# Performance work log

Hardware: AMD Instinct MI355X
Metric: run time of the kernel (lower is better)

Reference implementation:

```python
import jax, jax.numpy as jnp
import numpy as np

B, S, E = 2, 2048, 2048
H = 16
KV_RANK = 512
ROPE = 64
NOPE = 64  # source sets qk_nope_dim = qk_rope_dim
VD = 128   # v_head_dim = head_dim
QD = ROPE + NOPE  # q_head_dim = 128


def setup_inputs() -> dict:
    key = jax.random.key(0)
    ks = jax.random.split(key, 5)
    sd = lambda fan_in: 1.0 / np.sqrt(fan_in)
    return {
        "x": jax.random.normal(ks[0], (B, S, E), jnp.float32),
        "attention_mask": jnp.zeros((1, 1, S, S), jnp.float32),
        "W_kv_down": jax.random.normal(ks[1], (KV_RANK + ROPE, E), jnp.float32) * sd(E),
        "W_kv_up": jax.random.normal(ks[2], (H * (VD + NOPE), KV_RANK), jnp.float32) * sd(KV_RANK),
        "W_q": jax.random.normal(ks[3], (H * QD, E), jnp.float32) * sd(E),
        "W_out": jax.random.normal(ks[4], (E, H * VD), jnp.float32) * sd(H * VD),
    }


def reference(x, attention_mask, W_kv_down, W_kv_up, W_q, W_out):
    scale = QD ** (-0.5)
    # down-project to latent + rope part
    compressed = jnp.einsum('bse,fe->bsf', x, W_kv_down)          # [B,S,KV_RANK+ROPE]
    kv_c, k_rope = compressed[..., :KV_RANK], compressed[..., KV_RANK:]
    # up-project latent to per-head v and k_nope
    kv_exp = jnp.einsum('bsr,fr->bsf', kv_c, W_kv_up)             # [B,S,H*(VD+NOPE)]
    kv_exp = kv_exp.reshape(B, S, H, VD + NOPE).transpose(0, 2, 1, 3)  # [B,H,S,VD+NOPE]
    v, k_nope = kv_exp[..., :VD], kv_exp[..., VD:]
    # shared rope key broadcast over heads, concat [rope, nope]
    k_rope_b = jnp.broadcast_to(k_rope[:, None], (B, H, S, ROPE))
    k = jnp.concatenate([k_rope_b, k_nope], axis=-1)              # [B,H,S,QD]
    # queries
    q = jnp.einsum('bse,fe->bsf', x, W_q).reshape(B, S, H, QD).transpose(0, 2, 1, 3)
    scores = jnp.einsum('bhsd,bhtd->bhst', q, k) * scale + attention_mask
    w = jax.nn.softmax(scores, axis=-1)
    out = jnp.einsum('bhst,bhtv->bhsv', w, v)                     # [B,H,S,VD]
    out = out.transpose(0, 2, 1, 3).reshape(B, S, H * VD)
    return jnp.einsum('bsf,ef->bse', out, W_out)
```

## Files before the change

### kernel.cpp

```cpp
#include <hip/hip_runtime.h>
#include <hip/hip_bf16.h>
#include <stdint.h>

typedef __bf16 bf16x8 __attribute__((ext_vector_type(8)));
typedef float f32x4 __attribute__((ext_vector_type(4)));
typedef float f32x16 __attribute__((ext_vector_type(16)));
typedef uint32_t u32x4 __attribute__((ext_vector_type(4)));
typedef unsigned short ushort_t;
typedef unsigned short ushort8v __attribute__((ext_vector_type(8)));

#define MFMA16 __builtin_amdgcn_mfma_f32_16x16x32_bf16
#define MFMA32 __builtin_amdgcn_mfma_f32_32x32x16_bf16

static constexpr int Bc = 2, Sc = 2048, Ec = 2048, Hc = 16;

__device__ __forceinline__ void gload16(const void* g, void* l) {
  __builtin_amdgcn_global_load_lds(
      (const __attribute__((address_space(1))) void*)g,
      (__attribute__((address_space(3))) void*)l, 16, 0, 0);
}

__device__ __forceinline__ ushort_t f2bf(float f) {
  uint32_t u = __float_as_uint(f);
  uint32_t r = (u + 0x7fffu + ((u >> 16) & 1u)) >> 16;
  return (ushort_t)r;
}
__device__ __forceinline__ float bf2f(ushort_t u) {
  return __uint_as_float((uint32_t)u << 16);
}
__device__ __forceinline__ uint32_t cvtpk(float a, float b) {
  uint32_t d;
  asm("v_cvt_pk_bf16_f32 %0, %1, %2" : "=v"(d) : "v"(a), "v"(b));
  return d;
}
__device__ __forceinline__ void plswap(uint32_t& a, uint32_t& b) {
  asm("v_permlane32_swap_b32 %0, %1" : "+v"(a), "+v"(b));
}

__global__ void cast_all(const float* __restrict__ x, const float* __restrict__ Wq,
                         const float* __restrict__ Wkvu, const float* __restrict__ Wout,
                         const float* __restrict__ Wkvd,
                         ushort_t* __restrict__ xb, ushort_t* __restrict__ wq,
                         ushort_t* __restrict__ wkvu, ushort_t* __restrict__ wout,
                         ushort_t* __restrict__ wkvd) {
  int i = blockIdx.x * 256 + threadIdx.x;
  const float* src;
  ushort_t* dst;
  int j;
  if (i < 2097152) { src = x; dst = xb; j = i; }
  else if (i < 3145728) { src = Wq; dst = wq; j = i - 2097152; }
  else if (i < 3538944) { src = Wkvu; dst = wkvu; j = i - 3145728; }
  else if (i < 4587520) { src = Wout; dst = wout; j = i - 3538944; }
  else {
    j = i - 4587520;
    int row = j >> 9, col4 = j & 511;
    ushort4 o;
    if (row < 576) {
      float4 v = ((const float4*)Wkvd)[row * 512 + col4];
      o.x = f2bf(v.x); o.y = f2bf(v.y); o.z = f2bf(v.z); o.w = f2bf(v.w);
    } else { o.x = 0; o.y = 0; o.z = 0; o.w = 0; }
    ((ushort4*)wkvd)[j] = o;
    return;
  }
  float4 v = ((const float4*)src)[j];
  ushort4 o;
  o.x = f2bf(v.x); o.y = f2bf(v.y); o.z = f2bf(v.z); o.w = f2bf(v.w);
  ((ushort4*)dst)[j] = o;
}

__global__ void mask_rearrange(const float* __restrict__ mask, ushort_t* __restrict__ m4) {
  const float INVLN2 = 1.4426950408889634f;
  int i = blockIdx.x * 256 + threadIdx.x;
  if (i >= 524288) return;
  int rr = i & 1, half = (i >> 1) & 1, kblk = (i >> 2) & 1, kt = (i >> 3) & 31, q = i >> 8;
  const float* src = mask + (size_t)q * 2048 + kt * 64 + kblk * 32 + half * 4 + rr * 16;
  float4 a = *(const float4*)src;
  float4 c = *(const float4*)(src + 8);
  ushort8v o;
  o[0] = f2bf(a.x * INVLN2); o[1] = f2bf(a.y * INVLN2);
  o[2] = f2bf(a.z * INVLN2); o[3] = f2bf(a.w * INVLN2);
  o[4] = f2bf(c.x * INVLN2); o[5] = f2bf(c.y * INVLN2);
  o[6] = f2bf(c.z * INVLN2); o[7] = f2bf(c.w * INVLN2);
  ((ushort8v*)m4)[i] = o;
}

template<int MODE>
__global__ __launch_bounds__(256, 2)
void gemm_bt(const ushort_t* __restrict__ A, int lda,
             const ushort_t* __restrict__ Bm, int ldb,
             void* __restrict__ Cout, int ldc,
             int M, int N, int K,
             char* __restrict__ vtb, char* __restrict__ kbuf)
{
  __shared__ __align__(16) ushort_t sA[128 * 32];
  __shared__ __align__(16) ushort_t sB[128 * 32];
  int tid = threadIdx.x;
  int nTn = N >> 7;
  int bid = blockIdx.x;
  int chunk = gridDim.x >> 3;
  bid = (bid & 7) * chunk + (bid >> 3);
  int tm = bid / nTn, tn = bid - tm * nTn;
  int wave = tid >> 6, lane = tid & 63;
  int wm = (wave >> 1) << 6, wn = (wave & 1) << 6;
  int l16 = lane & 15, g16 = lane >> 4;
  f32x4 acc[4][4] = {};
  int srow = tid >> 2, scol = (tid & 3) << 3;
  const ushort_t* Ag = A + (size_t)(tm * 128 + srow) * lda + scol;
  const ushort_t* Bg = Bm + (size_t)(tn * 128 + srow) * ldb + scol;
  ushort_t* sAp = &sA[srow * 32 + scol];
  ushort_t* sBp = &sB[srow * 32 + scol];
  for (int kt = 0; kt < K; kt += 32) {
    gload16(Ag, sAp);
    gload16(Ag + (size_t)64 * lda, sAp + 64 * 32);
    gload16(Bg, sBp);
    gload16(Bg + (size_t)64 * ldb, sBp + 64 * 32);
    Ag += 32; Bg += 32;
    __syncthreads();
    bf16x8 af[4], bfr[4];
#pragma unroll
    for (int i = 0; i < 4; i++) af[i] = *(const bf16x8*)&sA[(wm + i * 16 + l16) * 32 + g16 * 8];
#pragma unroll
    for (int i = 0; i < 4; i++) bfr[i] = *(const bf16x8*)&sB[(wn + i * 16 + l16) * 32 + g16 * 8];
#pragma unroll
    for (int i = 0; i < 4; i++)
#pragma unroll
      for (int j = 0; j < 4; j++)
        acc[i][j] = MFMA16(af[i], bfr[j], acc[i][j], 0, 0, 0);
    __syncthreads();
  }
#pragma unroll
  for (int i = 0; i < 4; i++) {
#pragma unroll
    for (int j = 0; j < 4; j++) {
#pragma unroll
      for (int r = 0; r < 4; r++) {
        int grow = tm * 128 + wm + i * 16 + g16 * 4 + r;
        int gcol = tn * 128 + wn + j * 16 + l16;
        float v = acc[i][j][r];
        if constexpr (MODE == 0) {
          ((ushort_t*)Cout)[(size_t)grow * ldc + gcol] = f2bf(v);
        } else if constexpr (MODE == 2) {
          ((float*)Cout)[(size_t)grow * ldc + gcol] = v;
        } else {
          int h = gcol / 192, jj = gcol - h * 192;
          int b = grow >> 11, s = grow & 2047;
          size_t bh = (size_t)(b * Hc + h);
          if (jj < 128) {
            *(ushort_t*)(vtb + bh * 524288 + (size_t)jj * 4096 + ((s >> 6) * 128) +
                         ((2 * (s & 63)) ^ ((jj & 7) << 4))) = f2bf(v);
          } else {
            int col = 64 + (jj - 128);
            *(ushort_t*)(kbuf + (bh * Sc + s) * 256 + ((2 * col) ^ ((s & 7) << 4))) = f2bf(v);
          }
        }
      }
    }
  }
}

__global__ void rope_fill(const ushort_t* __restrict__ comp, char* __restrict__ kbuf) {
  int i = blockIdx.x * 256 + threadIdx.x;
  if (i >= Bc * Sc * 8) return;
  int blk = i & 7;
  int m = i >> 3;
  int s = m & 2047, b = m >> 11;
  uint4 v = *(const uint4*)&comp[(size_t)m * 640 + 512 + blk * 8];
  int off = (blk * 16) ^ ((s & 7) << 4);
#pragma unroll
  for (int h = 0; h < Hc; h++) {
    *(uint4*)(kbuf + ((size_t)(b * Hc + h) * Sc + s) * 256 + off) = v;
  }
}

__global__ __launch_bounds__(128, 2)
void attn_kernel(const ushort_t* __restrict__ qb, const char* __restrict__ kbuf,
                 const char* __restrict__ vtb, const ushort_t* __restrict__ m4,
                 ushort_t* __restrict__ attn_o)
{
  __shared__ __align__(16) char smem[32768];
  char* sK = smem;
  char* sV = smem + 16384;
  const float scale2 = 0.12752081738040466f;
  int bid = blockIdx.x;
  bid = (bid & 7) * 128 + (bid >> 3);
  int qt = bid & 31, bh = bid >> 5;
  int b = bh >> 4, h = bh & 15;
  int tid = threadIdx.x, wave = tid >> 6, lane = tid & 63;
  int l32 = lane & 31, half = lane >> 5;
  int sx = (l32 & 7) << 4;
  int qbase = qt * 64 + wave * 32;

  bf16x8 qf[8];
  {
    const ushort_t* qp = qb + (size_t)(b * Sc + qbase + l32) * 2048 + h * 128 + half * 8;
#pragma unroll
    for (int ks = 0; ks < 8; ks++) qf[ks] = *(const bf16x8*)(qp + ks * 16);
  }

  float mrun = -3.0e38f, lrun = 0.f;
  f32x16 acco[4] = {};

  const char* kg = kbuf + (size_t)bh * 524288;
  const char* vg = vtb + (size_t)bh * 524288;
  const ushort8v* mq = (const ushort8v*)m4 + (size_t)(qbase + l32) * 256 + half * 2;

  for (int kt = 0; kt < 32; kt++) {
#pragma unroll
    for (int it = 0; it < 8; it++)
      gload16(kg + kt * 16384 + it * 2048 + tid * 16, sK + it * 2048 + tid * 16);
#pragma unroll
    for (int it = 0; it < 8; it++) {
      int l = it * 2048 + tid * 16;
      gload16(vg + (size_t)(l >> 7) * 4096 + kt * 128 + (l & 127), sV + l);
    }
    ushort8v mvv[4];
#pragma unroll
    for (int kb = 0; kb < 2; kb++)
#pragma unroll
      for (int rr = 0; rr < 2; rr++)
        mvv[kb * 2 + rr] = mq[kt * 8 + kb * 4 + rr];
    __syncthreads();

#pragma unroll
    for (int kblk = 0; kblk < 2; kblk++) {
      f32x16 sc = {};
      __builtin_amdgcn_s_setprio(1);
#pragma unroll
      for (int ks = 0; ks < 8; ks++) {
        bf16x8 kfr = *(const bf16x8*)(sK + (kblk * 32 + l32) * 256 +
                                      ((ks * 32 + half * 16) ^ sx));
        sc = MFMA32(kfr, qf[ks], sc, 0, 0, 0);
      }
      __builtin_amdgcn_s_setprio(0);

#pragma unroll
      for (int r = 0; r < 16; r++)
        sc[r] = sc[r] * scale2 + bf2f(mvv[kblk * 2 + (r >> 3)][r & 7]);
      float mx = sc[0];
#pragma unroll
      for (int r = 1; r < 16; r++) mx = fmaxf(mx, sc[r]);
      mx = fmaxf(mx, __shfl_xor(mx, 32));
      if (!__all(mx <= mrun + 11.0f)) {
        float mnew = fmaxf(mrun, mx);
        float corr = __builtin_amdgcn_exp2f(mrun - mnew);
        lrun *= corr; mrun = mnew;
#pragma unroll
        for (int r = 0; r < 16; r++) {
          float cr = __shfl(corr, (r & 3) + 8 * (r >> 2) + 4 * half);
#pragma unroll
          for (int vb = 0; vb < 4; vb++) acco[vb][r] *= cr;
        }
      }
      float rs = 0.f;
      uint32_t W[8];
#pragma unroll
      for (int m = 0; m < 4; m++) {
        float p0 = __builtin_amdgcn_exp2f(sc[4 * m + 0] - mrun);
        float p1 = __builtin_amdgcn_exp2f(sc[4 * m + 1] - mrun);
        float p2 = __builtin_amdgcn_exp2f(sc[4 * m + 2] - mrun);
        float p3 = __builtin_amdgcn_exp2f(sc[4 * m + 3] - mrun);
        rs += (p0 + p1) + (p2 + p3);
        W[2 * m] = cvtpk(p0, p1);
        W[2 * m + 1] = cvtpk(p2, p3);
      }
      lrun += rs;

      bf16x8 pf[2];
#pragma unroll
      for (int k2 = 0; k2 < 2; k2++) {
        uint32_t a0 = W[4 * k2 + 0], a1 = W[4 * k2 + 1];
        uint32_t b0 = W[4 * k2 + 2], b1 = W[4 * k2 + 3];
        plswap(a0, b0);
        plswap(a1, b1);
        u32x4 t; t[0] = a0; t[1] = a1; t[2] = b0; t[3] = b1;
        pf[k2] = __builtin_bit_cast(bf16x8, t);
      }

      __builtin_amdgcn_s_setprio(1);
#pragma unroll
      for (int k2 = 0; k2 < 2; k2++)
#pragma unroll
        for (int vb = 0; vb < 4; vb++) {
          bf16x8 vf = *(const bf16x8*)(sV + (vb * 32 + l32) * 128 +
                                       ((kblk * 64 + k2 * 32 + half * 16) ^ sx));
          acco[vb] = MFMA32(pf[k2], vf, acco[vb], 0, 0, 0);
        }
      __builtin_amdgcn_s_setprio(0);
    }

    __syncthreads();
  }

  lrun += __shfl_xor(lrun, 32);
#pragma unroll
  for (int r = 0; r < 16; r++) {
    int rowq = (r & 3) + 8 * (r >> 2) + 4 * half;
    float lr = __shfl(lrun, rowq);
    float inv = 1.0f / lr;
    int qrow = qbase + rowq;
    ushort_t* op = attn_o + (size_t)(b * Sc + qrow) * 2048 + h * 128 + l32;
#pragma unroll
    for (int vb = 0; vb < 4; vb++)
      op[vb * 32] = f2bf(acco[vb][r] * inv);
  }
}

extern "C" void kernel_launch(void* const* d_in, const int* in_sizes, int n_in,
                              void* d_out, int out_size, void* d_ws, size_t ws_size,
                              hipStream_t stream) {
  const float* x    = (const float*)d_in[0];
  const float* mask = (const float*)d_in[1];
  const float* Wkvd = (const float*)d_in[2];
  const float* Wkvu = (const float*)d_in[3];
  const float* Wq   = (const float*)d_in[4];
  const float* Wout = (const float*)d_in[5];

  char* ws = (char*)d_ws;
  size_t off = 0;
  auto alloc = [&](size_t bytes) { char* p = ws + off; off += (bytes + 255) & ~(size_t)255; return p; };
  ushort_t* xb   = (ushort_t*)alloc((size_t)4096 * 2048 * 2);
  ushort_t* wkvd = (ushort_t*)alloc((size_t)640 * 2048 * 2);
  ushort_t* wq   = (ushort_t*)alloc((size_t)2048 * 2048 * 2);
  ushort_t* wkvu = (ushort_t*)alloc((size_t)3072 * 512 * 2);
  ushort_t* wout = (ushort_t*)alloc((size_t)2048 * 2048 * 2);
  ushort_t* comp = (ushort_t*)alloc((size_t)4096 * 640 * 2);
  ushort_t* qbuf = (ushort_t*)alloc((size_t)4096 * 2048 * 2);
  char*     kbuf = alloc((size_t)Bc * Hc * Sc * 256);
  char*     vtb  = alloc((size_t)Bc * Hc * 524288);
  ushort_t* attn_o = xb;
  ushort_t* m4 = wq;

  cast_all<<<19200, 256, 0, stream>>>(x, Wq, Wkvu, Wout, Wkvd, xb, wq, wkvu, wout, wkvd);

  gemm_bt<0><<<32 * 5, 256, 0, stream>>>(xb, 2048, wkvd, 2048, comp, 640, 4096, 640, 2048, nullptr, nullptr);
  gemm_bt<0><<<32 * 16, 256, 0, stream>>>(xb, 2048, wq, 2048, qbuf, 2048, 4096, 2048, 2048, nullptr, nullptr);
  mask_rearrange<<<2048, 256, 0, stream>>>(mask, m4);
  gemm_bt<1><<<32 * 24, 256, 0, stream>>>(comp, 640, wkvu, 512, nullptr, 0, 4096, 3072, 512, vtb, kbuf);
  rope_fill<<<32768 / 256, 256, 0, stream>>>(comp, kbuf);
  attn_kernel<<<1024, 128, 0, stream>>>(qbuf, kbuf, vtb, m4, attn_o);
  gemm_bt<2><<<32 * 16, 256, 0, stream>>>(attn_o, 2048, wout, 2048, d_out, 2048, 4096, 2048, 2048, nullptr, nullptr);
}
```

Baseline: 288.9 us.

## Double-buffer K/V tiles in LDS and process 64 keys per softmax step

The attention kernel now allocates two LDS buffers for K and V, so the async global-to-LDS load of the next tile is issued before computing on the current one, overlapping memory with MFMA work. The two 32-key sub-blocks are also merged into one online-softmax update per 64-key tile, halving the max/rescale passes. LDS use doubles to 64KB per block, which may cut occupancy from the requested 2 blocks per CU. The larger live register set from two score tiles also risks spills.

```diff
diff --git a/kernel.cpp b/kernel.cpp
--- a/kernel.cpp
+++ b/kernel.cpp
@@ -177,9 +177,11 @@
                  const char* __restrict__ vtb, const ushort_t* __restrict__ m4,
                  ushort_t* __restrict__ attn_o)
 {
-  __shared__ __align__(16) char smem[32768];
-  char* sK = smem;
-  char* sV = smem + 16384;
+  __shared__ __align__(16) char smem[65536];
+  char* sKA = smem;
+  char* sVA = smem + 16384;
+  char* sKB = smem + 32768;
+  char* sVB = smem + 49152;
   const float scale2 = 0.12752081738040466f;
   int bid = blockIdx.x;
   bid = (bid & 7) * 128 + (bid >> 3);
@@ -204,90 +206,120 @@
   const char* vg = vtb + (size_t)bh * 524288;
   const ushort8v* mq = (const ushort8v*)m4 + (size_t)(qbase + l32) * 256 + half * 2;
 
-  for (int kt = 0; kt < 32; kt++) {
+  auto STAGE = [&](int kt, char* sKb, char* sVb) {
 #pragma unroll
     for (int it = 0; it < 8; it++)
-      gload16(kg + kt * 16384 + it * 2048 + tid * 16, sK + it * 2048 + tid * 16);
+      gload16(kg + kt * 16384 + it * 2048 + tid * 16, sKb + it * 2048 + tid * 16);
 #pragma unroll
     for (int it = 0; it < 8; it++) {
       int l = it * 2048 + tid * 16;
-      gload16(vg + (size_t)(l >> 7) * 4096 + kt * 128 + (l & 127), sV + l);
-    }
+      gload16(vg + (size_t)(l >> 7) * 4096 + kt * 128 + (l & 127), sVb + l);
+    }
+  };
+
+  auto COMPUTE = [&](int kt, const char* sKb, const char* sVb) {
     ushort8v mvv[4];
 #pragma unroll
     for (int kb = 0; kb < 2; kb++)
 #pragma unroll
       for (int rr = 0; rr < 2; rr++)
         mvv[kb * 2 + rr] = mq[kt * 8 + kb * 4 + rr];
+
+    f32x16 sc0 = {}, sc1 = {};
+    __builtin_amdgcn_s_setprio(1);
+#pragma unroll
+    for (int ks = 0; ks < 8; ks++) {
+      bf16x8 k0 = *(const bf16x8*)(sKb + l32 * 256 + ((ks * 32 + half * 16) ^ sx));
+      bf16x8 k1 = *(const bf16x8*)(sKb + (32 + l32) * 256 + ((ks * 32 + half * 16) ^ sx));
+      sc0 = MFMA32(k0, qf[ks], sc0, 0, 0, 0);
+      sc1 = MFMA32(k1, qf[ks], sc1, 0, 0, 0);
+    }
+    __builtin_amdgcn_s_setprio(0);
+
+#pragma unroll
+    for (int r = 0; r < 16; r++) {
+      sc0[r] = sc0[r] * scale2 + bf2f(mvv[r >> 3][r & 7]);
+      sc1[r] = sc1[r] * scale2 + bf2f(mvv[2 + (r >> 3)][r & 7]);
+    }
+    float mx = fmaxf(sc0[0], sc1[0]);
+#pragma unroll
+    for (int r = 1; r < 16; r++) mx = fmaxf(mx, fmaxf(sc0[r], sc1[r]));
+    mx = fmaxf(mx, __shfl_xor(mx, 32));
+    if (!__all(mx <= mrun + 11.0f)) {
+      float mnew = fmaxf(mrun, mx);
+      float corr = __builtin_amdgcn_exp2f(mrun - mnew);
+      lrun *= corr; mrun = mnew;
+#pragma unroll
+      for (int r = 0; r < 16; r++) {
+        float cr = __shfl(corr, (r & 3) + 8 * (r >> 2) + 4 * half);
+#pragma unroll
+        for (int vb = 0; vb < 4; vb++) acco[vb][r] *= cr;
+      }
+    }
+    float rs = 0.f;
+    uint32_t W0[8], W1[8];
+#pragma unroll
+    for (int m = 0; m < 4; m++) {
+      float a0 = __builtin_amdgcn_exp2f(sc0[4 * m + 0] - mrun);
+      float a1 = __builtin_amdgcn_exp2f(sc0[4 * m + 1] - mrun);
+      float a2 = __builtin_amdgcn_exp2f(sc0[4 * m + 2] - mrun);
+      float a3 = __builtin_amdgcn_exp2f(sc0[4 * m + 3] - mrun);
+      float b0 = __builtin_amdgcn_exp2f(sc1[4 * m + 0] - mrun);
+      float b1 = __builtin_amdgcn_exp2f(sc1[4 * m + 1] - mrun);
+      float b2 = __builtin_amdgcn_exp2f(sc1[4 * m + 2] - mrun);
+      float b3 = __builtin_amdgcn_exp2f(sc1[4 * m + 3] - mrun);
+      rs += (a0 + a1) + (a2 + a3) + (b0 + b1) + (b2 + b3);
+      W0[2 * m] = cvtpk(a0, a1); W0[2 * m + 1] = cvtpk(a2, a3);
+      W1[2 * m] = cvtpk(b0, b1); W1[2 * m + 1] = cvtpk(b2, b3);
+    }
+    lrun += rs;
+
+    bf16x8 pf0[2], pf1[2];
+#pragma unroll
+    for (int k2 = 0; k2 < 2; k2++) {
+      {
+        uint32_t a0 = W0[4 * k2 + 0], a1 = W0[4 * k2 + 1];
+        uint32_t b0 = W0[4 * k2 + 2], b1 = W0[4 * k2 + 3];
+        plswap(a0, b0); plswap(a1, b1);
+        u32x4 t; t[0] = a0; t[1] = a1; t[2] = b0; t[3] = b1;
+        pf0[k2] = __builtin_bit_cast(bf16x8, t);
+      }
+      {
+        uint32_t a0 = W1[4 * k2 + 0], a1 = W1[4 * k2 + 1];
+        uint32_t b0 = W1[4 * k2 + 2], b1 = W1[4 * k2 + 3];
+        plswap(a0, b0); plswap(a1, b1);
+        u32x4 t; t[0] = a0; t[1] = a1; t[2] = b0; t[3] = b1;
+        pf1[k2] = __builtin_bit_cast(bf16x8, t);
+      }
+    }
+
+    __builtin_amdgcn_s_setprio(1);
+#pragma unroll
+    for (int k2 = 0; k2 < 2; k2++) {
+#pragma unroll
+      for (int vb = 0; vb < 4; vb++) {
+        bf16x8 vf = *(const bf16x8*)(sVb + (vb * 32 + l32) * 128 +
+                                     ((k2 * 32 + half * 16) ^ sx));
+        acco[vb] = MFMA32(pf0[k2], vf, acco[vb], 0, 0, 0);
+      }
+#pragma unroll
+      for (int vb = 0; vb < 4; vb++) {
+        bf16x8 vf = *(const bf16x8*)(sVb + (vb * 32 + l32) * 128 +
+                                     ((64 + k2 * 32 + half * 16) ^ sx));
+        acco[vb] = MFMA32(pf1[k2], vf, acco[vb], 0, 0, 0);
+      }
+    }
+    __builtin_amdgcn_s_setprio(0);
+  };
+
+  STAGE(0, sKA, sVA);
+  __syncthreads();
+  for (int kt = 0; kt < 32; kt += 2) {
+    STAGE(kt + 1, sKB, sVB);
+    COMPUTE(kt, sKA, sVA);
     __syncthreads();
-
-#pragma unroll
-    for (int kblk = 0; kblk < 2; kblk++) {
-      f32x16 sc = {};
-      __builtin_amdgcn_s_setprio(1);
-#pragma unroll
-      for (int ks = 0; ks < 8; ks++) {
-        bf16x8 kfr = *(const bf16x8*)(sK + (kblk * 32 + l32) * 256 +
-                                      ((ks * 32 + half * 16) ^ sx));
-        sc = MFMA32(kfr, qf[ks], sc, 0, 0, 0);
-      }
-      __builtin_amdgcn_s_setprio(0);
-
-#pragma unroll
-      for (int r = 0; r < 16; r++)
-        sc[r] = sc[r] * scale2 + bf2f(mvv[kblk * 2 + (r >> 3)][r & 7]);
-      float mx = sc[0];
-#pragma unroll
-      for (int r = 1; r < 16; r++) mx = fmaxf(mx, sc[r]);
-      mx = fmaxf(mx, __shfl_xor(mx, 32));
-      if (!__all(mx <= mrun + 11.0f)) {
-        float mnew = fmaxf(mrun, mx);
-        float corr = __builtin_amdgcn_exp2f(mrun - mnew);
-        lrun *= corr; mrun = mnew;
-#pragma unroll
-        for (int r = 0; r < 16; r++) {
-          float cr = __shfl(corr, (r & 3) + 8 * (r >> 2) + 4 * half);
-#pragma unroll
-          for (int vb = 0; vb < 4; vb++) acco[vb][r] *= cr;
-        }
-      }
-      float rs = 0.f;
-      uint32_t W[8];
-#pragma unroll
-      for (int m = 0; m < 4; m++) {
-        float p0 = __builtin_amdgcn_exp2f(sc[4 * m + 0] - mrun);
-        float p1 = __builtin_amdgcn_exp2f(sc[4 * m + 1] - mrun);
-        float p2 = __builtin_amdgcn_exp2f(sc[4 * m + 2] - mrun);
-        float p3 = __builtin_amdgcn_exp2f(sc[4 * m + 3] - mrun);
-        rs += (p0 + p1) + (p2 + p3);
-        W[2 * m] = cvtpk(p0, p1);
-        W[2 * m + 1] = cvtpk(p2, p3);
-      }
-      lrun += rs;
-
-      bf16x8 pf[2];
-#pragma unroll
-      for (int k2 = 0; k2 < 2; k2++) {
-        uint32_t a0 = W[4 * k2 + 0], a1 = W[4 * k2 + 1];
-        uint32_t b0 = W[4 * k2 + 2], b1 = W[4 * k2 + 3];
-        plswap(a0, b0);
-        plswap(a1, b1);
-        u32x4 t; t[0] = a0; t[1] = a1; t[2] = b0; t[3] = b1;
-        pf[k2] = __builtin_bit_cast(bf16x8, t);
-      }
-
-      __builtin_amdgcn_s_setprio(1);
-#pragma unroll
-      for (int k2 = 0; k2 < 2; k2++)
-#pragma unroll
-        for (int vb = 0; vb < 4; vb++) {
-          bf16x8 vf = *(const bf16x8*)(sV + (vb * 32 + l32) * 128 +
-                                       ((kblk * 64 + k2 * 32 + half * 16) ^ sx));
-          acco[vb] = MFMA32(pf[k2], vf, acco[vb], 0, 0, 0);
-        }
-      __builtin_amdgcn_s_setprio(0);
-    }
-
+    if (kt + 2 < 32) STAGE(kt + 2, sKA, sVA);
+    COMPUTE(kt + 1, sKB, sVB);
     __syncthreads();
   }
 
```

Result: slower. 311.1 us (+7.7%).

## Process two 32-row query blocks per wave in attention to reuse K/V tiles

Applied to the files above, without the earlier changes.

Each attention wave now handles 64 query rows (two independent 32-row accumulators) instead of 32, so each block covers 128 queries and the grid halves to 512 blocks. Every K and V fragment read from shared memory feeds two MFMAs, which halves the global-to-LDS traffic and LDS reads per unit of work. In exchange register pressure roughly doubles, so launch bounds drop to one block per SM hint. Fewer blocks and fewer resident waves may expose more latency and leave the GPU underfilled.

```diff
diff --git a/kernel.cpp b/kernel.cpp
--- a/kernel.cpp
+++ b/kernel.cpp
@@ -172,7 +172,7 @@
   }
 }
 
-__global__ __launch_bounds__(128, 2)
+__global__ __launch_bounds__(128, 1)
 void attn_kernel(const ushort_t* __restrict__ qb, const char* __restrict__ kbuf,
                  const char* __restrict__ vtb, const ushort_t* __restrict__ m4,
                  ushort_t* __restrict__ attn_o)
@@ -182,27 +182,34 @@
   char* sV = smem + 16384;
   const float scale2 = 0.12752081738040466f;
   int bid = blockIdx.x;
-  bid = (bid & 7) * 128 + (bid >> 3);
-  int qt = bid & 31, bh = bid >> 5;
+  bid = (bid & 7) * 64 + (bid >> 3);
+  int qt = bid & 15, bh = bid >> 4;
   int b = bh >> 4, h = bh & 15;
   int tid = threadIdx.x, wave = tid >> 6, lane = tid & 63;
   int l32 = lane & 31, half = lane >> 5;
   int sx = (l32 & 7) << 4;
-  int qbase = qt * 64 + wave * 32;
-
-  bf16x8 qf[8];
+  int qbase = qt * 128 + wave * 64;
+
+  bf16x8 qf0[8], qf1[8];
   {
-    const ushort_t* qp = qb + (size_t)(b * Sc + qbase + l32) * 2048 + h * 128 + half * 8;
-#pragma unroll
-    for (int ks = 0; ks < 8; ks++) qf[ks] = *(const bf16x8*)(qp + ks * 16);
-  }
-
-  float mrun = -3.0e38f, lrun = 0.f;
-  f32x16 acco[4] = {};
+    const ushort_t* qp0 = qb + (size_t)(b * Sc + qbase + l32) * 2048 + h * 128 + half * 8;
+    const ushort_t* qp1 = qp0 + (size_t)32 * 2048;
+#pragma unroll
+    for (int ks = 0; ks < 8; ks++) {
+      qf0[ks] = *(const bf16x8*)(qp0 + ks * 16);
+      qf1[ks] = *(const bf16x8*)(qp1 + ks * 16);
+    }
+  }
+
+  float mrun0 = -3.0e38f, lrun0 = 0.f;
+  float mrun1 = -3.0e38f, lrun1 = 0.f;
+  f32x16 acc0[4] = {}, acc1[4] = {};
 
   const char* kg = kbuf + (size_t)bh * 524288;
   const char* vg = vtb + (size_t)bh * 524288;
-  const ushort8v* mq = (const ushort8v*)m4 + (size_t)(qbase + l32) * 256 + half * 2;
+  const ushort8v* mqb = (const ushort8v*)m4;
+  size_t mo0 = (size_t)(qbase + l32) * 256 + half * 2;
+  size_t mo1 = mo0 + (size_t)32 * 256;
 
   for (int kt = 0; kt < 32; kt++) {
 #pragma unroll
@@ -213,67 +220,96 @@
       int l = it * 2048 + tid * 16;
       gload16(vg + (size_t)(l >> 7) * 4096 + kt * 128 + (l & 127), sV + l);
     }
-    ushort8v mvv[4];
-#pragma unroll
-    for (int kb = 0; kb < 2; kb++)
-#pragma unroll
-      for (int rr = 0; rr < 2; rr++)
-        mvv[kb * 2 + rr] = mq[kt * 8 + kb * 4 + rr];
     __syncthreads();
 
 #pragma unroll
     for (int kblk = 0; kblk < 2; kblk++) {
-      f32x16 sc = {};
+      ushort8v mv00 = mqb[mo0 + kt * 8 + kblk * 4 + 0];
+      ushort8v mv01 = mqb[mo0 + kt * 8 + kblk * 4 + 1];
+      ushort8v mv10 = mqb[mo1 + kt * 8 + kblk * 4 + 0];
+      ushort8v mv11 = mqb[mo1 + kt * 8 + kblk * 4 + 1];
+
+      f32x16 sc0 = {}, sc1 = {};
       __builtin_amdgcn_s_setprio(1);
 #pragma unroll
       for (int ks = 0; ks < 8; ks++) {
         bf16x8 kfr = *(const bf16x8*)(sK + (kblk * 32 + l32) * 256 +
                                       ((ks * 32 + half * 16) ^ sx));
-        sc = MFMA32(kfr, qf[ks], sc, 0, 0, 0);
+        sc0 = MFMA32(kfr, qf0[ks], sc0, 0, 0, 0);
+        sc1 = MFMA32(kfr, qf1[ks], sc1, 0, 0, 0);
       }
       __builtin_amdgcn_s_setprio(0);
 
 #pragma unroll
-      for (int r = 0; r < 16; r++)
-        sc[r] = sc[r] * scale2 + bf2f(mvv[kblk * 2 + (r >> 3)][r & 7]);
-      float mx = sc[0];
-#pragma unroll
-      for (int r = 1; r < 16; r++) mx = fmaxf(mx, sc[r]);
-      mx = fmaxf(mx, __shfl_xor(mx, 32));
-      if (!__all(mx <= mrun + 11.0f)) {
-        float mnew = fmaxf(mrun, mx);
-        float corr = __builtin_amdgcn_exp2f(mrun - mnew);
-        lrun *= corr; mrun = mnew;
+      for (int r = 0; r < 16; r++) {
+        sc0[r] = sc0[r] * scale2 + bf2f((r < 8 ? mv00 : mv01)[r & 7]);
+        sc1[r] = sc1[r] * scale2 + bf2f((r < 8 ? mv10 : mv11)[r & 7]);
+      }
+      float mx0 = sc0[0], mx1 = sc1[0];
+#pragma unroll
+      for (int r = 1; r < 16; r++) { mx0 = fmaxf(mx0, sc0[r]); mx1 = fmaxf(mx1, sc1[r]); }
+      mx0 = fmaxf(mx0, __shfl_xor(mx0, 32));
+      mx1 = fmaxf(mx1, __shfl_xor(mx1, 32));
+      bool ok = (mx0 <= mrun0 + 11.0f) & (mx1 <= mrun1 + 11.0f);
+      if (!__all(ok)) {
+        float mnew0 = fmaxf(mrun0, mx0), mnew1 = fmaxf(mrun1, mx1);
+        float corr0 = __builtin_amdgcn_exp2f(mrun0 - mnew0);
+        float corr1 = __builtin_amdgcn_exp2f(mrun1 - mnew1);
+        lrun0 *= corr0; mrun0 = mnew0;
+        lrun1 *= corr1; mrun1 = mnew1;
 #pragma unroll
         for (int r = 0; r < 16; r++) {
-          float cr = __shfl(corr, (r & 3) + 8 * (r >> 2) + 4 * half);
-#pragma unroll
-          for (int vb = 0; vb < 4; vb++) acco[vb][r] *= cr;
-        }
-      }
-      float rs = 0.f;
-      uint32_t W[8];
-#pragma unroll
-      for (int m = 0; m < 4; m++) {
-        float p0 = __builtin_amdgcn_exp2f(sc[4 * m + 0] - mrun);
-        float p1 = __builtin_amdgcn_exp2f(sc[4 * m + 1] - mrun);
-        float p2 = __builtin_amdgcn_exp2f(sc[4 * m + 2] - mrun);
-        float p3 = __builtin_amdgcn_exp2f(sc[4 * m + 3] - mrun);
-        rs += (p0 + p1) + (p2 + p3);
-        W[2 * m] = cvtpk(p0, p1);
-        W[2 * m + 1] = cvtpk(p2, p3);
-      }
-      lrun += rs;
-
-      bf16x8 pf[2];
-#pragma unroll
-      for (int k2 = 0; k2 < 2; k2++) {
-        uint32_t a0 = W[4 * k2 + 0], a1 = W[4 * k2 + 1];
-        uint32_t b0 = W[4 * k2 + 2], b1 = W[4 * k2 + 3];
-        plswap(a0, b0);
-        plswap(a1, b1);
-        u32x4 t; t[0] = a0; t[1] = a1; t[2] = b0; t[3] = b1;
-        pf[k2] = __builtin_bit_cast(bf16x8, t);
+          int rowq = (r & 3) + 8 * (r >> 2) + 4 * half;
+          float cr0 = __shfl(corr0, rowq);
+          float cr1 = __shfl(corr1, rowq);
+#pragma unroll
+          for (int vb = 0; vb < 4; vb++) { acc0[vb][r] *= cr0; acc1[vb][r] *= cr1; }
+        }
+      }
+      bf16x8 pf0[2], pf1[2];
+      {
+        float rs = 0.f;
+        uint32_t W[8];
+#pragma unroll
+        for (int m = 0; m < 4; m++) {
+          float p0 = __builtin_amdgcn_exp2f(sc0[4 * m + 0] - mrun0);
+          float p1 = __builtin_amdgcn_exp2f(sc0[4 * m + 1] - mrun0);
+          float p2 = __builtin_amdgcn_exp2f(sc0[4 * m + 2] - mrun0);
+          float p3 = __builtin_amdgcn_exp2f(sc0[4 * m + 3] - mrun0);
+          rs += (p0 + p1) + (p2 + p3);
+          W[2 * m] = cvtpk(p0, p1); W[2 * m + 1] = cvtpk(p2, p3);
+        }
+        lrun0 += rs;
+#pragma unroll
+        for (int k2 = 0; k2 < 2; k2++) {
+          uint32_t a0 = W[4 * k2 + 0], a1 = W[4 * k2 + 1];
+          uint32_t b0 = W[4 * k2 + 2], b1 = W[4 * k2 + 3];
+          plswap(a0, b0); plswap(a1, b1);
+          u32x4 t; t[0] = a0; t[1] = a1; t[2] = b0; t[3] = b1;
+          pf0[k2] = __builtin_bit_cast(bf16x8, t);
+        }
+      }
+      {
+        float rs = 0.f;
+        uint32_t W[8];
+#pragma unroll
+        for (int m = 0; m < 4; m++) {
+          float p0 = __builtin_amdgcn_exp2f(sc1[4 * m + 0] - mrun1);
+          float p1 = __builtin_amdgcn_exp2f(sc1[4 * m + 1] - mrun1);
+          float p2 = __builtin_amdgcn_exp2f(sc1[4 * m + 2] - mrun1);
+          float p3 = __builtin_amdgcn_exp2f(sc1[4 * m + 3] - mrun1);
+          rs += (p0 + p1) + (p2 + p3);
+          W[2 * m] = cvtpk(p0, p1); W[2 * m + 1] = cvtpk(p2, p3);
+        }
+        lrun1 += rs;
+#pragma unroll
+        for (int k2 = 0; k2 < 2; k2++) {
+          uint32_t a0 = W[4 * k2 + 0], a1 = W[4 * k2 + 1];
+          uint32_t b0 = W[4 * k2 + 2], b1 = W[4 * k2 + 3];
+          plswap(a0, b0); plswap(a1, b1);
+          u32x4 t; t[0] = a0; t[1] = a1; t[2] = b0; t[3] = b1;
+          pf1[k2] = __builtin_bit_cast(bf16x8, t);
+        }
       }
 
       __builtin_amdgcn_s_setprio(1);
@@ -283,7 +319,8 @@
         for (int vb = 0; vb < 4; vb++) {
           bf16x8 vf = *(const bf16x8*)(sV + (vb * 32 + l32) * 128 +
                                        ((kblk * 64 + k2 * 32 + half * 16) ^ sx));
-          acco[vb] = MFMA32(pf[k2], vf, acco[vb], 0, 0, 0);
+          acc0[vb] = MFMA32(pf0[k2], vf, acc0[vb], 0, 0, 0);
+          acc1[vb] = MFMA32(pf1[k2], vf, acc1[vb], 0, 0, 0);
         }
       __builtin_amdgcn_s_setprio(0);
     }
@@ -291,17 +328,20 @@
     __syncthreads();
   }
 
-  lrun += __shfl_xor(lrun, 32);
+  lrun0 += __shfl_xor(lrun0, 32);
+  lrun1 += __shfl_xor(lrun1, 32);
 #pragma unroll
   for (int r = 0; r < 16; r++) {
     int rowq = (r & 3) + 8 * (r >> 2) + 4 * half;
-    float lr = __shfl(lrun, rowq);
-    float inv = 1.0f / lr;
-    int qrow = qbase + rowq;
-    ushort_t* op = attn_o + (size_t)(b * Sc + qrow) * 2048 + h * 128 + l32;
-#pragma unroll
-    for (int vb = 0; vb < 4; vb++)
-      op[vb * 32] = f2bf(acco[vb][r] * inv);
+    float inv0 = 1.0f / __shfl(lrun0, rowq);
+    float inv1 = 1.0f / __shfl(lrun1, rowq);
+    ushort_t* op0 = attn_o + (size_t)(b * Sc + qbase + rowq) * 2048 + h * 128 + l32;
+    ushort_t* op1 = op0 + (size_t)32 * 2048;
+#pragma unroll
+    for (int vb = 0; vb < 4; vb++) {
+      op0[vb * 32] = f2bf(acc0[vb][r] * inv0);
+      op1[vb * 32] = f2bf(acc1[vb][r] * inv1);
+    }
   }
 }
 
@@ -337,6 +377,6 @@
   mask_rearrange<<<2048, 256, 0, stream>>>(mask, m4);
   gemm_bt<1><<<32 * 24, 256, 0, stream>>>(comp, 640, wkvu, 512, nullptr, 0, 4096, 3072, 512, vtb, kbuf);
   rope_fill<<<32768 / 256, 256, 0, stream>>>(comp, kbuf);
-  attn_kernel<<<1024, 128, 0, stream>>>(qbuf, kbuf, vtb, m4, attn_o);
+  attn_kernel<<<512, 128, 0, stream>>>(qbuf, kbuf, vtb, m4, attn_o);
   gemm_bt<2><<<32 * 16, 256, 0, stream>>>(attn_o, 2048, wout, 2048, d_out, 2048, 4096, 2048, 2048, nullptr, nullptr);
 }
```

Measured after the change: 299.5 us. 1.04x slower.
